# Performance work log

Measured on AMD Instinct MI355X. Metric: run time of the kernel, lower is better.

## Reference

```python
import jax, jax.numpy as jnp
import numpy as np

N_NODES = 50000
N_EDGES = 800000
IN_CH = 128
OUT_CH = 64
HEADS = 1
NEG_SLOPE = 0.2

def _glorot(key, shape):
    stdv = np.sqrt(6.0 / (shape[-2] + shape[-1]))
    return jax.random.uniform(key, shape, jnp.float32, -stdv, stdv)

def setup_inputs() -> dict:
    key = jax.random.key(0)
    k1, k2, k3, k4, k5 = jax.random.split(key, 5)
    x = jax.random.normal(k1, (N_NODES, IN_CH), jnp.float32)
    src = jax.random.randint(k2, (N_EDGES,), 0, N_NODES)
    dst = jax.random.randint(k3, (N_EDGES,), 0, N_NODES)
    # ensure no pre-existing self loops (remove_self_loops is then identity)
    dst = jnp.where(src == dst, (dst + 1) % N_NODES, dst)
    edge_index = jnp.stack([src, dst]).astype(jnp.int64)
    weight = _glorot(k4, (IN_CH, HEADS * OUT_CH))
    att = _glorot(k5, (1, HEADS, 2 * OUT_CH))
    bias = jnp.zeros((OUT_CH,), jnp.float32)
    return {"x": x, "edge_index": edge_index, "weight": weight, "att": att, "bias": bias}

def reference(x, edge_index, weight, att, bias):
    N = x.shape[0]
    # linear projection -> [N, heads, out]
    h = (x @ weight).reshape(N, HEADS, OUT_CH)
    # add self loops (input guaranteed free of self loops)
    loops = jnp.arange(N, dtype=edge_index.dtype)
    src = jnp.concatenate([edge_index[0], loops])  # source j
    dst = jnp.concatenate([edge_index[1], loops])  # target i
    x_j = h[src]   # [E+N, heads, out]
    x_i = h[dst]
    # attention logits: (cat([x_i, x_j]) * att).sum(-1) -> [E+N, heads]
    alpha = jnp.concatenate([x_i, x_j], axis=-1)
    alpha = (alpha * att).sum(axis=-1)
    alpha = jax.nn.leaky_relu(alpha, NEG_SLOPE)
    # segment softmax over destination nodes
    amax = jax.ops.segment_max(alpha, dst, num_segments=N)
    e = jnp.exp(alpha - amax[dst])
    esum = jax.ops.segment_sum(e, dst, num_segments=N)
    alpha = e / (esum[dst] + 1e-16)
    # message + scatter-add aggregation
    msg = x_j * alpha[:, :, None]
    out = jax.ops.segment_sum(msg, dst, num_segments=N)  # [N, heads, out]
    out = out.mean(axis=1) + bias
    # F.normalize (L2, dim=1, eps=1e-12); dropout is eval-mode identity
    norm = jnp.maximum(jnp.linalg.norm(out, axis=1, keepdims=True), 1e-12)
    return out / norm
```

## Files before the change

kernel.cpp:

```cpp
#include <hip/hip_runtime.h>
#include <math.h>

#define IN_CH 128
#define OUT_CH 64
#define NEG_SLOPE 0.2f

__device__ __forceinline__ unsigned short f2bf(float f) {
    unsigned u = __float_as_uint(f);
    unsigned r = (u + 0x7FFFu + ((u >> 16) & 1u)) >> 16;
    return (unsigned short)r;
}

__device__ __forceinline__ bool sniff_is64(const void* edges) {
    const unsigned* up = (const unsigned*)edges;
    bool is64 = true;
#pragma unroll
    for (int k = 0; k < 16; k++) is64 = is64 && (up[2 * k + 1] == 0u);
    return is64;
}

__global__ __launch_bounds__(256) void k_mm_count(
        const float* __restrict__ x, const float* __restrict__ W,
        const float* __restrict__ att, unsigned short* __restrict__ h16,
        float* __restrict__ asrc, float* __restrict__ adst, int N,
        const void* __restrict__ edges, int* __restrict__ counts,
        unsigned short* __restrict__ rank, int E, int mmb, int cntb) {
    __shared__ float Ws[IN_CH * OUT_CH];
    int t = threadIdx.x;
    int bid = blockIdx.x;
    int lo = min(mmb, cntb), M2 = 2 * lo;
    int role, id;
    if (bid < M2) { role = bid & 1; id = bid >> 1; }
    else          { role = (mmb > cntb) ? 0 : 1; id = bid - M2 + lo; }

    if (role == 1) {
        int e0 = (id * 256 + t) * 4;
        if (e0 >= E) return;
        int d[4];
        if (sniff_is64(edges)) {
            const long long* p = (const long long*)edges;
            if (e0 + 3 < E) {
                int4 v0 = *(const int4*)&p[(size_t)E + e0];
                int4 v1 = *(const int4*)&p[(size_t)E + e0 + 2];
                d[0] = v0.x; d[1] = v0.z; d[2] = v1.x; d[3] = v1.z;
            } else {
                for (int i = 0; i < 4; i++)
                    d[i] = (e0 + i < E) ? (int)p[(size_t)E + e0 + i] : 0;
            }
        } else {
            const int* p = (const int*)edges;
            if (e0 + 3 < E) {
                int4 v = *(const int4*)&p[E + e0];
                d[0] = v.x; d[1] = v.y; d[2] = v.z; d[3] = v.w;
            } else {
                for (int i = 0; i < 4; i++)
                    d[i] = (e0 + i < E) ? p[E + e0 + i] : 0;
            }
        }
        if (e0 + 3 < E) {
            ushort4 r;
            r.x = (unsigned short)atomicAdd(counts + d[0], 1);
            r.y = (unsigned short)atomicAdd(counts + d[1], 1);
            r.z = (unsigned short)atomicAdd(counts + d[2], 1);
            r.w = (unsigned short)atomicAdd(counts + d[3], 1);
            *(ushort4*)&rank[e0] = r;
        } else {
            for (int i = 0; i < 4; i++)
                if (e0 + i < E)
                    rank[e0 + i] = (unsigned short)atomicAdd(counts + d[i], 1);
        }
        return;
    }

    for (int i = t * 4; i < IN_CH * OUT_CH; i += 256 * 4)
        *(float4*)&Ws[i] = *(const float4*)&W[i];
    int cg = t & 15, g = t >> 4;
    float4 att_d = *(const float4*)&att[cg * 4];
    float4 att_s = *(const float4*)&att[64 + cg * 4];
    __syncthreads();

    int n0 = id * 64 + g * 4;
    int nn[4];
#pragma unroll
    for (int m = 0; m < 4; m++) nn[m] = min(n0 + m, N - 1);

    float4 acc[4];
#pragma unroll
    for (int m = 0; m < 4; m++) acc[m] = make_float4(0.f, 0.f, 0.f, 0.f);

#pragma unroll 2
    for (int k4 = 0; k4 < IN_CH / 4; k4++) {
        float4 xv[4];
#pragma unroll
        for (int m = 0; m < 4; m++)
            xv[m] = *(const float4*)&x[(size_t)nn[m] * IN_CH + k4 * 4];
        float4 wv[4];
#pragma unroll
        for (int j = 0; j < 4; j++)
            wv[j] = *(const float4*)&Ws[(k4 * 4 + j) * OUT_CH + cg * 4];
#pragma unroll
        for (int m = 0; m < 4; m++) {
            acc[m].x = fmaf(xv[m].x, wv[0].x, acc[m].x);
            acc[m].y = fmaf(xv[m].x, wv[0].y, acc[m].y);
            acc[m].z = fmaf(xv[m].x, wv[0].z, acc[m].z);
            acc[m].w = fmaf(xv[m].x, wv[0].w, acc[m].w);
            acc[m].x = fmaf(xv[m].y, wv[1].x, acc[m].x);
            acc[m].y = fmaf(xv[m].y, wv[1].y, acc[m].y);
            acc[m].z = fmaf(xv[m].y, wv[1].z, acc[m].z);
            acc[m].w = fmaf(xv[m].y, wv[1].w, acc[m].w);
            acc[m].x = fmaf(xv[m].z, wv[2].x, acc[m].x);
            acc[m].y = fmaf(xv[m].z, wv[2].y, acc[m].y);
            acc[m].z = fmaf(xv[m].z, wv[2].z, acc[m].z);
            acc[m].w = fmaf(xv[m].z, wv[2].w, acc[m].w);
            acc[m].x = fmaf(xv[m].w, wv[3].x, acc[m].x);
            acc[m].y = fmaf(xv[m].w, wv[3].y, acc[m].y);
            acc[m].z = fmaf(xv[m].w, wv[3].z, acc[m].z);
            acc[m].w = fmaf(xv[m].w, wv[3].w, acc[m].w);
        }
    }

#pragma unroll
    for (int m = 0; m < 4; m++) {
        int node = n0 + m;
        if (node < N) {
            ushort4 hv;
            hv.x = f2bf(acc[m].x);
            hv.y = f2bf(acc[m].y);
            hv.z = f2bf(acc[m].z);
            hv.w = f2bf(acc[m].w);
            *(ushort4*)&h16[(size_t)node * OUT_CH + cg * 4] = hv;
        }
        float pd = acc[m].x * att_d.x + acc[m].y * att_d.y +
                   acc[m].z * att_d.z + acc[m].w * att_d.w;
        float ps = acc[m].x * att_s.x + acc[m].y * att_s.y +
                   acc[m].z * att_s.z + acc[m].w * att_s.w;
#pragma unroll
        for (int msk = 1; msk < 16; msk <<= 1) {
            pd += __shfl_xor(pd, msk, 64);
            ps += __shfl_xor(ps, msk, 64);
        }
        if (cg == 0 && node < N) { adst[node] = pd; asrc[node] = ps; }
    }
}

__global__ __launch_bounds__(256) void k_scanA(const int* __restrict__ counts,
                                               int* __restrict__ partials, int N) {
    __shared__ int red[256];
    int t = threadIdx.x;
    int base = blockIdx.x * 1024 + t * 4;
    int s = 0;
    if (base + 3 < N) {
        int4 v = *(const int4*)(counts + base);
        s = v.x + v.y + v.z + v.w;
    } else {
        for (int i = 0; i < 4; i++) if (base + i < N) s += counts[base + i];
    }
    red[t] = s;
    __syncthreads();
    for (int off = 128; off > 0; off >>= 1) {
        if (t < off) red[t] += red[t + off];
        __syncthreads();
    }
    if (t == 0) partials[blockIdx.x] = red[0];
}

__global__ __launch_bounds__(256) void k_scanC(const int* __restrict__ counts,
                                               const int* __restrict__ partials,
                                               int nb, int total,
                                               int* __restrict__ rowptr, int N) {
    __shared__ int shp[256];
    __shared__ int sh[256];
    int t = threadIdx.x;
    shp[t] = (t < nb) ? partials[t] : 0;
    __syncthreads();
    for (int off = 1; off < 256; off <<= 1) {
        int v = (t >= off) ? shp[t - off] : 0;
        __syncthreads();
        shp[t] += v;
        __syncthreads();
    }
    int base_blk = (blockIdx.x == 0) ? 0 : shp[blockIdx.x - 1];

    int base = blockIdx.x * 1024 + t * 4;
    int c[4];
    int s = 0;
#pragma unroll
    for (int i = 0; i < 4; i++) {
        int idx = base + i;
        c[i] = (idx < N) ? counts[idx] : 0;
        s += c[i];
    }
    sh[t] = s;
    __syncthreads();
    for (int off = 1; off < 256; off <<= 1) {
        int v = (t >= off) ? sh[t - off] : 0;
        __syncthreads();
        sh[t] += v;
        __syncthreads();
    }
    int run = ((t == 0) ? 0 : sh[t - 1]) + base_blk;
#pragma unroll
    for (int i = 0; i < 4; i++) {
        int idx = base + i;
        if (idx < N) {
            rowptr[idx] = run;
            run += c[i];
        }
    }
    if (blockIdx.x == 0 && t == 0) rowptr[N] = total;
}

__global__ void k_scatter(const void* __restrict__ edges,
                          const unsigned short* __restrict__ rank,
                          const int* __restrict__ rowptr,
                          int* __restrict__ csr_src, int E) {
    int e0 = (blockIdx.x * blockDim.x + threadIdx.x) * 4;
    if (e0 >= E) return;
    int s[4], d[4];
    if (e0 + 3 < E) {
        if (sniff_is64(edges)) {
            const long long* p = (const long long*)edges;
            int4 a0 = *(const int4*)&p[e0];
            int4 a1 = *(const int4*)&p[e0 + 2];
            int4 b0 = *(const int4*)&p[(size_t)E + e0];
            int4 b1 = *(const int4*)&p[(size_t)E + e0 + 2];
            s[0] = a0.x; s[1] = a0.z; s[2] = a1.x; s[3] = a1.z;
            d[0] = b0.x; d[1] = b0.z; d[2] = b1.x; d[3] = b1.z;
        } else {
            const int* p = (const int*)edges;
            int4 a = *(const int4*)&p[e0];
            int4 b = *(const int4*)&p[E + e0];
            s[0] = a.x; s[1] = a.y; s[2] = a.z; s[3] = a.w;
            d[0] = b.x; d[1] = b.y; d[2] = b.z; d[3] = b.w;
        }
        ushort4 r = *(const ushort4*)&rank[e0];
        csr_src[rowptr[d[0]] + r.x] = s[0];
        csr_src[rowptr[d[1]] + r.y] = s[1];
        csr_src[rowptr[d[2]] + r.z] = s[2];
        csr_src[rowptr[d[3]] + r.w] = s[3];
    } else {
        bool is64 = sniff_is64(edges);
        for (int i = 0; i < 4; i++) {
            if (e0 + i >= E) break;
            int sv, dv;
            if (is64) {
                const long long* p = (const long long*)edges;
                sv = (int)p[e0 + i];
                dv = (int)p[(size_t)E + e0 + i];
            } else {
                const int* p = (const int*)edges;
                sv = p[e0 + i];
                dv = p[E + e0 + i];
            }
            csr_src[rowptr[dv] + rank[e0 + i]] = sv;
        }
    }
}

__global__ __launch_bounds__(256) void k_agg(const unsigned short* __restrict__ h16,
                                             const int* __restrict__ csr_src,
                                             const int* __restrict__ rowptr,
                                             const float* __restrict__ asrc,
                                             const float* __restrict__ adst,
                                             const float* __restrict__ bias,
                                             float* __restrict__ out, int N) {
    __shared__ float2 stage[4][64];
    int lane = threadIdx.x & 63;
    int wid = threadIdx.x >> 6;
    int node = blockIdx.x * 4 + wid;
    if (node >= N) return;
    int half = lane >> 5;
    int ch2 = (lane & 31) * 2;

    float aD = adst[node];
    float a = aD + asrc[node];
    a = a > 0.f ? a : NEG_SLOPE * a;
    float w_self = __expf(a);
    unsigned hv = *(const unsigned*)&h16[(size_t)node * OUT_CH + ch2];
    float wse = half ? 0.f : w_self;
    float accx = wse * __uint_as_float(hv << 16);
    float accy = wse * __uint_as_float(hv & 0xFFFF0000u);
    float esum_lane = 0.f;

    int b0 = rowptr[node], b1 = rowptr[node + 1];
    for (int base = b0; base < b1; base += 64) {
        int idx = base + lane;
        int sv = 0;
        float wv = 0.f;
        if (idx < b1) {
            sv = csr_src[idx];
            float av = aD + asrc[sv];
            av = av > 0.f ? av : NEG_SLOPE * av;
            wv = __expf(av);
        }
        esum_lane += wv;
        stage[wid][lane] = make_float2(__int_as_float(sv), wv);

        int n = min(64, b1 - base);
        for (int j = 0; j < n; j += 16) {
#pragma unroll
            for (int k = 0; k < 8; k++) {
                float2 p = stage[wid][j + 2 * k + half];
                int s = __float_as_int(p.x);
                unsigned v = *(const unsigned*)&h16[((size_t)s << 6) + ch2];
                accx = fmaf(p.y, __uint_as_float(v << 16), accx);
                accy = fmaf(p.y, __uint_as_float(v & 0xFFFF0000u), accy);
            }
        }
    }
    accx += __shfl_xor(accx, 32, 64);
    accy += __shfl_xor(accy, 32, 64);
#pragma unroll
    for (int m = 32; m >= 1; m >>= 1) esum_lane += __shfl_xor(esum_lane, m, 64);
    float esum = esum_lane + w_self;

    float inv = 1.f / (esum + 1e-16f);
    float2 bv = *(const float2*)&bias[ch2];
    float vx = accx * inv + bv.x;
    float vy = accy * inv + bv.y;
    float ss = vx * vx + vy * vy;
#pragma unroll
    for (int m = 16; m >= 1; m >>= 1) ss += __shfl_xor(ss, m, 64);
    float rinv = 1.f / fmaxf(sqrtf(ss), 1e-12f);
    if (!half)
        *(float2*)&out[(size_t)node * OUT_CH + ch2] = make_float2(vx * rinv, vy * rinv);
}

extern "C" void kernel_launch(void* const* d_in, const int* in_sizes, int n_in,
                              void* d_out, int out_size, void* d_ws, size_t ws_size,
                              hipStream_t stream) {
    const float* x    = (const float*)d_in[0];
    const void*  edges = d_in[1];
    const float* W    = (const float*)d_in[2];
    const float* att  = (const float*)d_in[3];
    const float* bias = (const float*)d_in[4];
    float* out = (float*)d_out;

    const int N = in_sizes[0] / IN_CH;
    const int E = in_sizes[1] / 2;
    const int NB = (N + 1023) / 1024;
    const int MMB = (N + 63) / 64;
    const int CNTB = (E + 1023) / 1024;

    char* ws = (char*)d_ws;
    size_t off = 0;
    auto alloc = [&](size_t bytes) -> void* {
        void* p = ws + off;
        off += bytes;
        off = (off + 255) & ~(size_t)255;
        return p;
    };
    int*            counts   = (int*)alloc((size_t)N * 4);
    int*            rowptr   = (int*)alloc((size_t)(N + 1) * 4);
    unsigned short* rank     = (unsigned short*)alloc((size_t)E * 2);
    int*            partials = (int*)alloc((size_t)256 * 4);
    unsigned short* h16      = (unsigned short*)alloc((size_t)N * OUT_CH * 2);
    float*          asrc     = (float*)alloc((size_t)N * 4);
    float*          adst     = (float*)alloc((size_t)N * 4);
    int*            csr_src  = (int*)alloc((size_t)E * 4);

    hipMemsetAsync(counts, 0, (size_t)N * 4, stream);
    k_mm_count<<<MMB + CNTB, 256, 0, stream>>>(x, W, att, h16, asrc, adst, N,
                                               edges, counts, rank, E, MMB, CNTB);
    k_scanA<<<NB, 256, 0, stream>>>(counts, partials, N);
    k_scanC<<<NB, 256, 0, stream>>>(counts, partials, NB, E, rowptr, N);
    k_scatter<<<(E + 1023) / 1024, 256, 0, stream>>>(edges, rank, rowptr,
                                                     csr_src, E);
    k_agg<<<(N + 3) / 4, 256, 0, stream>>>(h16, csr_src, rowptr, asrc, adst,
                                           bias, out, N);
}
```

Before: 160.2 us.

## Replace CSR build with fixed-capacity per-node slot buckets plus overflow list

Result: faster. 143.4 us (-10.5%).

```diff
diff --git a/kernel.cpp b/kernel.cpp
--- a/kernel.cpp
+++ b/kernel.cpp
@@ -4,6 +4,7 @@
 #define IN_CH 128
 #define OUT_CH 64
 #define NEG_SLOPE 0.2f
+#define CAP 64
 
 __device__ __forceinline__ unsigned short f2bf(float f) {
     unsigned u = __float_as_uint(f);
@@ -19,55 +20,74 @@
     return is64;
 }
 
-__global__ __launch_bounds__(256) void k_mm_count(
+__global__ __launch_bounds__(256) void k_mm_cs(
         const float* __restrict__ x, const float* __restrict__ W,
         const float* __restrict__ att, unsigned short* __restrict__ h16,
         float* __restrict__ asrc, float* __restrict__ adst, int N,
         const void* __restrict__ edges, int* __restrict__ counts,
-        unsigned short* __restrict__ rank, int E, int mmb, int cntb) {
+        int* __restrict__ slots, int* __restrict__ oflow_cnt,
+        int2* __restrict__ oflow, int E, int mmb, int csb) {
     __shared__ float Ws[IN_CH * OUT_CH];
     int t = threadIdx.x;
     int bid = blockIdx.x;
-    int lo = min(mmb, cntb), M2 = 2 * lo;
+    int lo = min(mmb, csb), M2 = 2 * lo;
     int role, id;
     if (bid < M2) { role = bid & 1; id = bid >> 1; }
-    else          { role = (mmb > cntb) ? 0 : 1; id = bid - M2 + lo; }
+    else          { role = (mmb > csb) ? 0 : 1; id = bid - M2 + lo; }
 
     if (role == 1) {
         int e0 = (id * 256 + t) * 4;
         if (e0 >= E) return;
-        int d[4];
-        if (sniff_is64(edges)) {
-            const long long* p = (const long long*)edges;
-            if (e0 + 3 < E) {
-                int4 v0 = *(const int4*)&p[(size_t)E + e0];
-                int4 v1 = *(const int4*)&p[(size_t)E + e0 + 2];
-                d[0] = v0.x; d[1] = v0.z; d[2] = v1.x; d[3] = v1.z;
+        int s[4], d[4];
+        bool full = (e0 + 3 < E);
+        if (full) {
+            if (sniff_is64(edges)) {
+                const long long* p = (const long long*)edges;
+                int4 a0 = *(const int4*)&p[e0];
+                int4 a1 = *(const int4*)&p[e0 + 2];
+                int4 b0 = *(const int4*)&p[(size_t)E + e0];
+                int4 b1 = *(const int4*)&p[(size_t)E + e0 + 2];
+                s[0] = a0.x; s[1] = a0.z; s[2] = a1.x; s[3] = a1.z;
+                d[0] = b0.x; d[1] = b0.z; d[2] = b1.x; d[3] = b1.z;
             } else {
-                for (int i = 0; i < 4; i++)
-                    d[i] = (e0 + i < E) ? (int)p[(size_t)E + e0 + i] : 0;
+                const int* p = (const int*)edges;
+                int4 a = *(const int4*)&p[e0];
+                int4 b = *(const int4*)&p[E + e0];
+                s[0] = a.x; s[1] = a.y; s[2] = a.z; s[3] = a.w;
+                d[0] = b.x; d[1] = b.y; d[2] = b.z; d[3] = b.w;
+            }
+#pragma unroll
+            for (int i = 0; i < 4; i++) {
+                int r = atomicAdd(counts + d[i], 1);
+                if (r < CAP) {
+                    slots[((size_t)d[i] << 6) + r] = s[i];
+                } else {
+                    int p = atomicAdd(oflow_cnt, 1);
+                    oflow[p] = make_int2(s[i], d[i]);
+                }
             }
         } else {
-            const int* p = (const int*)edges;
-            if (e0 + 3 < E) {
-                int4 v = *(const int4*)&p[E + e0];
-                d[0] = v.x; d[1] = v.y; d[2] = v.z; d[3] = v.w;
-            } else {
-                for (int i = 0; i < 4; i++)
-                    d[i] = (e0 + i < E) ? p[E + e0 + i] : 0;
-            }
-        }
-        if (e0 + 3 < E) {
-            ushort4 r;
-            r.x = (unsigned short)atomicAdd(counts + d[0], 1);
-            r.y = (unsigned short)atomicAdd(counts + d[1], 1);
-            r.z = (unsigned short)atomicAdd(counts + d[2], 1);
-            r.w = (unsigned short)atomicAdd(counts + d[3], 1);
-            *(ushort4*)&rank[e0] = r;
-        } else {
-            for (int i = 0; i < 4; i++)
-                if (e0 + i < E)
-                    rank[e0 + i] = (unsigned short)atomicAdd(counts + d[i], 1);
+            bool is64 = sniff_is64(edges);
+            for (int i = 0; i < 4; i++) {
+                if (e0 + i >= E) break;
+                int sv, dv;
+                if (is64) {
+                    const long long* p = (const long long*)edges;
+                    sv = (int)p[e0 + i];
+                    dv = (int)p[(size_t)E + e0 + i];
+                } else {
+                    const int* p = (const int*)edges;
+                    sv = p[e0 + i];
+                    dv = p[E + e0 + i];
+                }
+                int r = atomicAdd(counts + dv, 1);
+                if (r < CAP) {
+                    slots[((size_t)dv << 6) + r] = sv;
+                } else {
+                    int p2 = atomicAdd(oflow_cnt, 1);
+                    oflow[p2] = make_int2(sv, dv);
+                }
+            }
         }
         return;
     }
@@ -143,123 +163,11 @@
     }
 }
 
-__global__ __launch_bounds__(256) void k_scanA(const int* __restrict__ counts,
-                                               int* __restrict__ partials, int N) {
-    __shared__ int red[256];
-    int t = threadIdx.x;
-    int base = blockIdx.x * 1024 + t * 4;
-    int s = 0;
-    if (base + 3 < N) {
-        int4 v = *(const int4*)(counts + base);
-        s = v.x + v.y + v.z + v.w;
-    } else {
-        for (int i = 0; i < 4; i++) if (base + i < N) s += counts[base + i];
-    }
-    red[t] = s;
-    __syncthreads();
-    for (int off = 128; off > 0; off >>= 1) {
-        if (t < off) red[t] += red[t + off];
-        __syncthreads();
-    }
-    if (t == 0) partials[blockIdx.x] = red[0];
-}
-
-__global__ __launch_bounds__(256) void k_scanC(const int* __restrict__ counts,
-                                               const int* __restrict__ partials,
-                                               int nb, int total,
-                                               int* __restrict__ rowptr, int N) {
-    __shared__ int shp[256];
-    __shared__ int sh[256];
-    int t = threadIdx.x;
-    shp[t] = (t < nb) ? partials[t] : 0;
-    __syncthreads();
-    for (int off = 1; off < 256; off <<= 1) {
-        int v = (t >= off) ? shp[t - off] : 0;
-        __syncthreads();
-        shp[t] += v;
-        __syncthreads();
-    }
-    int base_blk = (blockIdx.x == 0) ? 0 : shp[blockIdx.x - 1];
-
-    int base = blockIdx.x * 1024 + t * 4;
-    int c[4];
-    int s = 0;
-#pragma unroll
-    for (int i = 0; i < 4; i++) {
-        int idx = base + i;
-        c[i] = (idx < N) ? counts[idx] : 0;
-        s += c[i];
-    }
-    sh[t] = s;
-    __syncthreads();
-    for (int off = 1; off < 256; off <<= 1) {
-        int v = (t >= off) ? sh[t - off] : 0;
-        __syncthreads();
-        sh[t] += v;
-        __syncthreads();
-    }
-    int run = ((t == 0) ? 0 : sh[t - 1]) + base_blk;
-#pragma unroll
-    for (int i = 0; i < 4; i++) {
-        int idx = base + i;
-        if (idx < N) {
-            rowptr[idx] = run;
-            run += c[i];
-        }
-    }
-    if (blockIdx.x == 0 && t == 0) rowptr[N] = total;
-}
-
-__global__ void k_scatter(const void* __restrict__ edges,
-                          const unsigned short* __restrict__ rank,
-                          const int* __restrict__ rowptr,
-                          int* __restrict__ csr_src, int E) {
-    int e0 = (blockIdx.x * blockDim.x + threadIdx.x) * 4;
-    if (e0 >= E) return;
-    int s[4], d[4];
-    if (e0 + 3 < E) {
-        if (sniff_is64(edges)) {
-            const long long* p = (const long long*)edges;
-            int4 a0 = *(const int4*)&p[e0];
-            int4 a1 = *(const int4*)&p[e0 + 2];
-            int4 b0 = *(const int4*)&p[(size_t)E + e0];
-            int4 b1 = *(const int4*)&p[(size_t)E + e0 + 2];
-            s[0] = a0.x; s[1] = a0.z; s[2] = a1.x; s[3] = a1.z;
-            d[0] = b0.x; d[1] = b0.z; d[2] = b1.x; d[3] = b1.z;
-        } else {
-            const int* p = (const int*)edges;
-            int4 a = *(const int4*)&p[e0];
-            int4 b = *(const int4*)&p[E + e0];
-            s[0] = a.x; s[1] = a.y; s[2] = a.z; s[3] = a.w;
-            d[0] = b.x; d[1] = b.y; d[2] = b.z; d[3] = b.w;
-        }
-        ushort4 r = *(const ushort4*)&rank[e0];
-        csr_src[rowptr[d[0]] + r.x] = s[0];
-        csr_src[rowptr[d[1]] + r.y] = s[1];
-        csr_src[rowptr[d[2]] + r.z] = s[2];
-        csr_src[rowptr[d[3]] + r.w] = s[3];
-    } else {
-        bool is64 = sniff_is64(edges);
-        for (int i = 0; i < 4; i++) {
-            if (e0 + i >= E) break;
-            int sv, dv;
-            if (is64) {
-                const long long* p = (const long long*)edges;
-                sv = (int)p[e0 + i];
-                dv = (int)p[(size_t)E + e0 + i];
-            } else {
-                const int* p = (const int*)edges;
-                sv = p[e0 + i];
-                dv = p[E + e0 + i];
-            }
-            csr_src[rowptr[dv] + rank[e0 + i]] = sv;
-        }
-    }
-}
-
 __global__ __launch_bounds__(256) void k_agg(const unsigned short* __restrict__ h16,
-                                             const int* __restrict__ csr_src,
-                                             const int* __restrict__ rowptr,
+                                             const int* __restrict__ slots,
+                                             const int* __restrict__ counts,
+                                             const int* __restrict__ oflow_cnt,
+                                             const int2* __restrict__ oflow,
                                              const float* __restrict__ asrc,
                                              const float* __restrict__ adst,
                                              const float* __restrict__ bias,
@@ -282,30 +190,27 @@
     float accy = wse * __uint_as_float(hv & 0xFFFF0000u);
     float esum_lane = 0.f;
 
-    int b0 = rowptr[node], b1 = rowptr[node + 1];
-    for (int base = b0; base < b1; base += 64) {
-        int idx = base + lane;
-        int sv = 0;
-        float wv = 0.f;
-        if (idx < b1) {
-            sv = csr_src[idx];
-            float av = aD + asrc[sv];
-            av = av > 0.f ? av : NEG_SLOPE * av;
-            wv = __expf(av);
-        }
-        esum_lane += wv;
-        stage[wid][lane] = make_float2(__int_as_float(sv), wv);
-
-        int n = min(64, b1 - base);
-        for (int j = 0; j < n; j += 16) {
-#pragma unroll
-            for (int k = 0; k < 8; k++) {
-                float2 p = stage[wid][j + 2 * k + half];
-                int s = __float_as_int(p.x);
-                unsigned v = *(const unsigned*)&h16[((size_t)s << 6) + ch2];
-                accx = fmaf(p.y, __uint_as_float(v << 16), accx);
-                accy = fmaf(p.y, __uint_as_float(v & 0xFFFF0000u), accy);
-            }
+    int c = counts[node];
+    int cs = min(c, CAP);
+    int sv = 0;
+    float wv = 0.f;
+    if (lane < cs) {
+        sv = slots[((size_t)node << 6) + lane];
+        float av = aD + asrc[sv];
+        av = av > 0.f ? av : NEG_SLOPE * av;
+        wv = __expf(av);
+    }
+    esum_lane = wv;
+    stage[wid][lane] = make_float2(__int_as_float(sv), wv);
+
+    for (int j = 0; j < cs; j += 16) {
+#pragma unroll
+        for (int k = 0; k < 8; k++) {
+            float2 p = stage[wid][j + 2 * k + half];
+            int s = __float_as_int(p.x);
+            unsigned v = *(const unsigned*)&h16[((size_t)s << 6) + ch2];
+            accx = fmaf(p.y, __uint_as_float(v << 16), accx);
+            accy = fmaf(p.y, __uint_as_float(v & 0xFFFF0000u), accy);
         }
     }
     accx += __shfl_xor(accx, 32, 64);
@@ -313,6 +218,22 @@
 #pragma unroll
     for (int m = 32; m >= 1; m >>= 1) esum_lane += __shfl_xor(esum_lane, m, 64);
     float esum = esum_lane + w_self;
+
+    int oc = *oflow_cnt;
+    if (oc > 0) {
+        for (int i = 0; i < oc; i++) {
+            int2 e = oflow[i];
+            if (e.y == node) {
+                float av = aD + asrc[e.x];
+                av = av > 0.f ? av : NEG_SLOPE * av;
+                float w = __expf(av);
+                esum += w;
+                unsigned v = *(const unsigned*)&h16[((size_t)e.x << 6) + ch2];
+                accx = fmaf(w, __uint_as_float(v << 16), accx);
+                accy = fmaf(w, __uint_as_float(v & 0xFFFF0000u), accy);
+            }
+        }
+    }
 
     float inv = 1.f / (esum + 1e-16f);
     float2 bv = *(const float2*)&bias[ch2];
@@ -338,9 +259,8 @@
 
     const int N = in_sizes[0] / IN_CH;
     const int E = in_sizes[1] / 2;
-    const int NB = (N + 1023) / 1024;
     const int MMB = (N + 63) / 64;
-    const int CNTB = (E + 1023) / 1024;
+    const int CSB = (E + 1023) / 1024;
 
     char* ws = (char*)d_ws;
     size_t off = 0;
@@ -350,22 +270,18 @@
         off = (off + 255) & ~(size_t)255;
         return p;
     };
-    int*            counts   = (int*)alloc((size_t)N * 4);
-    int*            rowptr   = (int*)alloc((size_t)(N + 1) * 4);
-    unsigned short* rank     = (unsigned short*)alloc((size_t)E * 2);
-    int*            partials = (int*)alloc((size_t)256 * 4);
+    int*            counts   = (int*)alloc((size_t)(N + 64) * 4);
+    int*            slots    = (int*)alloc((size_t)N * CAP * 4);
+    int2*           oflow    = (int2*)alloc((size_t)E * 8);
     unsigned short* h16      = (unsigned short*)alloc((size_t)N * OUT_CH * 2);
     float*          asrc     = (float*)alloc((size_t)N * 4);
     float*          adst     = (float*)alloc((size_t)N * 4);
-    int*            csr_src  = (int*)alloc((size_t)E * 4);
-
-    hipMemsetAsync(counts, 0, (size_t)N * 4, stream);
-    k_mm_count<<<MMB + CNTB, 256, 0, stream>>>(x, W, att, h16, asrc, adst, N,
-                                               edges, counts, rank, E, MMB, CNTB);
-    k_scanA<<<NB, 256, 0, stream>>>(counts, partials, N);
-    k_scanC<<<NB, 256, 0, stream>>>(counts, partials, NB, E, rowptr, N);
-    k_scatter<<<(E + 1023) / 1024, 256, 0, stream>>>(edges, rank, rowptr,
-                                                     csr_src, E);
-    k_agg<<<(N + 3) / 4, 256, 0, stream>>>(h16, csr_src, rowptr, asrc, adst,
-                                           bias, out, N);
-}
+    int*            oflow_cnt = counts + N;
+
+    hipMemsetAsync(counts, 0, (size_t)(N + 64) * 4, stream);
+    k_mm_cs<<<MMB + CSB, 256, 0, stream>>>(x, W, att, h16, asrc, adst, N,
+                                           edges, counts, slots, oflow_cnt,
+                                           oflow, E, MMB, CSB);
+    k_agg<<<(N + 3) / 4, 256, 0, stream>>>(h16, slots, counts, oflow_cnt, oflow,
+                                           asrc, adst, bias, out, N);
+}
```
